# Kernel tuning notes

Measured on AMD Instinct MI355X. Metric: run time of the kernel, lower is better.

Reference implementation:

```python
import jax, jax.numpy as jnp
import numpy as np

EPS = 1e-5
SLOPE = 0.1


def _leaky(v):
    return jnp.where(v >= 0, v, SLOPE * v)


def _bn(v, gamma, beta):
    # v: (C, Q, k); training-mode batch norm over (Q, k) with biased variance
    m = v.mean(axis=(1, 2), keepdims=True)
    var = v.var(axis=(1, 2), keepdims=True)
    return (v - m) * jax.lax.rsqrt(var + EPS) * gamma[:, None, None] + beta[:, None, None]


def setup_inputs() -> dict:
    key = jax.random.key(0)
    ks = jax.random.split(key, 6)
    Q, S, K, F, O = 16384, 16384, 32, 64, 64
    q_points = jax.random.normal(ks[0], (Q, 3), dtype=jnp.float32)
    s_points = jax.random.normal(ks[1], (S, 3), dtype=jnp.float32)
    neighb_inds = jax.random.randint(ks[2], (Q, K), 0, S + 1)  # S is the padded zero row
    feat = jax.random.normal(ks[3], (S, F), dtype=jnp.float32)
    conv0_w = jax.random.normal(ks[4], (O, F), dtype=jnp.float32) * 0.1
    conv1_w = jax.random.normal(ks[5], (O * 3, O), dtype=jnp.float32) * 0.1
    return {
        "q_points": q_points,
        "s_points": s_points,
        "feat": feat,
        "neighb_inds": neighb_inds,
        "conv0_w": conv0_w,
        "gamma0": jnp.ones((O,), jnp.float32),
        "beta0": jnp.zeros((O,), jnp.float32),
        "conv1_w": conv1_w,
        "gamma1": jnp.ones((O,), jnp.float32),
        "beta1": jnp.zeros((O,), jnp.float32),
    }


def reference(q_points, s_points, feat, neighb_inds, conv0_w, gamma0, beta0, conv1_w, gamma1, beta1):
    Q, K = neighb_inds.shape
    n_supports = s_points.shape[0]
    out_c = conv1_w.shape[1]
    in_c = conv1_w.shape[0] // out_c  # = 3 for feat_mode='xyz'

    # pad with a zero row (index n_supports is the 'out of range' shadow point)
    s_pad = jnp.concatenate([s_points, jnp.zeros((1, s_points.shape[1]), s_points.dtype)], 0)
    f_pad = jnp.concatenate([feat, jnp.zeros((1, feat.shape[1]), feat.dtype)], 0)

    # relative xyz feature; zero out shadow neighbors
    x = s_pad[neighb_inds] - q_points[:, None, :]          # (Q, K, 3)
    mask = (neighb_inds == n_supports)[..., None]
    x = jnp.where(mask, jnp.zeros((), x.dtype), x)

    y = f_pad[neighb_inds]                                  # (Q, K, F)

    # kernel generation: conv0 (1x1) -> BN -> LeakyReLU -> conv1 (1x1)
    h = jnp.einsum('of,qkf->oqk', conv0_w, y)               # (O, Q, K)
    h = _leaky(_bn(h, gamma0, beta0))
    ker = jnp.einsum('co,oqk->qkc', conv1_w, h)             # (Q, K, O*in_c)
    ker = ker.reshape(Q, K, out_c, in_c)                    # (Q, K, O, 3)

    # per-edge matmul against relative xyz, then BN -> LeakyReLU -> max over k
    z = jnp.einsum('qkoi,qki->oqk', ker, x)                 # (O, Q, K)
    z = _leaky(_bn(z, gamma1, beta1))
    z = z.max(axis=2)                                       # (O, Q)
    return z.T                                              # (Q, O)
```

## Files before the change

### kernel.cpp

```cpp
#include <hip/hip_runtime.h>
#include <hip/hip_bf16.h>

typedef __attribute__((ext_vector_type(8))) short bf16x8;
typedef __attribute__((ext_vector_type(4))) float f32x4;

constexpr int Q = 16384, S = 16384, KNN = 32, F = 64, O = 64;
constexpr int NEDGE = Q * KNN;
constexpr int QB = 8;
constexpr int EB = 256;
constexpr int GD = Q / QB;
constexpr int GH = 256;
constexpr float EPSV = 1e-5f;

constexpr size_t CNT_OFF   = 0;
constexpr size_t CTR_OFF   = 65536;
constexpr size_t P0_OFF    = 65600;
constexpr size_t ST0_OFF   = P0_OFF + (size_t)GH * 128 * 4;
constexpr size_t ZMIN_OFF  = ST0_OFF + 512;
constexpr size_t P1_OFF    = ZMIN_OFF + (size_t)Q * O * 4;
constexpr size_t ST1_OFF   = P1_OFF + (size_t)GD * 128 * 4;
constexpr size_t W0F_OFF   = ST1_OFF + 512;
constexpr size_t W1F_OFF   = W0F_OFF + 8192;
constexpr size_t FEATB_OFF = W1F_OFF + 24576;

__device__ __forceinline__ short f2bf(float f) {
  __hip_bfloat16 h = __float2bfloat16(f);
  short r; __builtin_memcpy(&r, &h, 2); return r;
}

__global__ void k_prep_hist(const float* __restrict__ w0g, const float* __restrict__ w1g,
                            short* __restrict__ w0f, short* __restrict__ w1f,
                            const float* __restrict__ feat, short* __restrict__ featb,
                            const int* __restrict__ inds, int* __restrict__ cnt) {
  __shared__ int lh[S];
  const int bx = blockIdx.x, tt = threadIdx.x;
  if (bx < 8) {
    const int t = bx * 256 + tt;
    const int fa = t >> 6, ln = t & 63;
    const int l4 = ln >> 4, l15 = ln & 15;
    if (fa < 8) {
      const int mt = fa >> 1, kk = fa & 1;
      const int o = 16 * mt + l15, f = 32 * kk + 8 * l4;
      const float* src = w0g + o * 64 + f;
      bf16x8 pk;
#pragma unroll
      for (int j = 0; j < 8; ++j) pk[j] = f2bf(src[j]);
      *(bf16x8*)&w0f[t * 8] = pk;
    } else {
      const int fb = fa - 8;
      const int nt = fb >> 1, kk = fb & 1;
      const int i = nt >> 2, b = nt & 3;
      const int o = 16 * b + l15;
      const float* row = w1g + (o * 3 + i) * 64;
      const int base = 32 * kk + 4 * l4;
      bf16x8 pk;
#pragma unroll
      for (int j = 0; j < 4; ++j) pk[j] = f2bf(row[base + j]);
#pragma unroll
      for (int j = 4; j < 8; ++j) pk[j] = f2bf(row[base + 16 + (j & 3)]);
      *(bf16x8*)&w1f[(fb * 64 + ln) * 8] = pk;
    }
  } else if (bx < 72) {
    const int base = (bx - 8) * 16384;
#pragma unroll
    for (int j = 0; j < 8; ++j) {
      const int i = base + j * 2048 + tt * 8;
      f32x4 a = *(const f32x4*)(feat + i);
      f32x4 b = *(const f32x4*)(feat + i + 4);
      bf16x8 pk;
      pk[0] = f2bf(a[0]); pk[1] = f2bf(a[1]); pk[2] = f2bf(a[2]); pk[3] = f2bf(a[3]);
      pk[4] = f2bf(b[0]); pk[5] = f2bf(b[1]); pk[6] = f2bf(b[2]); pk[7] = f2bf(b[3]);
      *(bf16x8*)(featb + i) = pk;
    }
  } else {
    for (int c = tt; c < S; c += 256) lh[c] = 0;
    __syncthreads();
    const int4* ip = (const int4*)inds;
    const int base = (bx - 72) * 2048;
#pragma unroll
    for (int j = 0; j < 8; ++j) {
      const int4 v = ip[base + j * 256 + tt];
      if (v.x < S) atomicAdd(&lh[v.x], 1);
      if (v.y < S) atomicAdd(&lh[v.y], 1);
      if (v.z < S) atomicAdd(&lh[v.z], 1);
      if (v.w < S) atomicAdd(&lh[v.w], 1);
    }
    __syncthreads();
    for (int c = tt; c < S; c += 256) {
      const int v = lh[c];
      if (v) atomicAdd(&cnt[c], v);
    }
  }
}

__global__ void k_hsq(const short* __restrict__ featb, const int* __restrict__ cnt,
                      const short* __restrict__ w0f, float* __restrict__ p0,
                      int* __restrict__ ctr, const float* __restrict__ g0,
                      const float* __restrict__ b0, float* __restrict__ st0) {
  __shared__ float sred[4][2][64];
  __shared__ int isLast;
  const int t = threadIdx.x, blk = blockIdx.x;
  const int wv = t >> 6, ln = t & 63, l4 = ln >> 4, l15 = ln & 15;

  const bf16x8* w0v = (const bf16x8*)w0f;
  bf16x8 w0a[8];
#pragma unroll
  for (int fa = 0; fa < 8; ++fa) w0a[fa] = w0v[fa * 64 + ln];

  const int s0 = blk * 64 + wv * 16;
  const float wc = (float)cnt[s0 + l15];
  const short* fb = featb + (size_t)(s0 + l15) * F + 8 * l4;
  const bf16x8 y0 = *(const bf16x8*)(fb);
  const bf16x8 y1 = *(const bf16x8*)(fb + 32);

  float hs[4][4], hq[4][4];
#pragma unroll
  for (int mt = 0; mt < 4; ++mt) {
    f32x4 acc = {0.f, 0.f, 0.f, 0.f};
    acc = __builtin_amdgcn_mfma_f32_16x16x32_bf16(w0a[2 * mt], y0, acc, 0, 0, 0);
    acc = __builtin_amdgcn_mfma_f32_16x16x32_bf16(w0a[2 * mt + 1], y1, acc, 0, 0, 0);
#pragma unroll
    for (int r = 0; r < 4; ++r) {
      const float h = acc[r];
      hs[mt][r] = wc * h;
      hq[mt][r] = wc * h * h;
    }
  }
#pragma unroll
  for (int mt = 0; mt < 4; ++mt)
#pragma unroll
    for (int r = 0; r < 4; ++r) {
      float s = hs[mt][r], q = hq[mt][r];
#pragma unroll
      for (int d = 1; d < 16; d <<= 1) { s += __shfl_xor(s, d); q += __shfl_xor(q, d); }
      hs[mt][r] = s; hq[mt][r] = q;
    }
  if (l15 == 0) {
#pragma unroll
    for (int mt = 0; mt < 4; ++mt)
#pragma unroll
      for (int r = 0; r < 4; ++r) {
        const int o = 16 * mt + 4 * l4 + r;
        sred[wv][0][o] = hs[mt][r];
        sred[wv][1][o] = hq[mt][r];
      }
  }
  __syncthreads();
  if (t < 128) {
    const int qq = t >> 6, o = t & 63;
    p0[(size_t)blk * 128 + t] =
        sred[0][qq][o] + sred[1][qq][o] + sred[2][qq][o] + sred[3][qq][o];
  }
  __syncthreads();
  __threadfence();
  if (t == 0) isLast = (atomicAdd(&ctr[0], 1) == GH - 1);
  __syncthreads();
  if (isLast) {
    __threadfence();
    if (t < O) {
      float s = 0.f, q = 0.f;
      for (int b = 0; b < GH; ++b) {
        s += p0[(size_t)b * 128 + t];
        q += p0[(size_t)b * 128 + 64 + t];
      }
      const float invN = 1.f / (float)NEDGE;
      const float mean = s * invN;
      const float var = q * invN - mean * mean;
      const float sc = g0[t] * rsqrtf(var + EPSV);
      st0[t] = sc;
      st0[O + t] = b0[t] - mean * sc;
    }
  }
}

__launch_bounds__(256, 2)
__global__ void k_main(const float* __restrict__ qpts, const float* __restrict__ spts,
                       const short* __restrict__ featb, const int* __restrict__ inds,
                       const short* __restrict__ w0f, const short* __restrict__ w1f,
                       const float* __restrict__ st0,
                       float* __restrict__ zmax, float* __restrict__ zmin,
                       float* __restrict__ p1) {
  __shared__ __align__(16) float xs[3 * EB];
  __shared__ float swred[512];

  const int t = threadIdx.x, blk = blockIdx.x;
  const int wv = t >> 6, ln = t & 63, l4 = ln >> 4, l15 = ln & 15;
  const int ebase = blk * EB;

  const int idx0 = inds[ebase + t];
  {
    const int q = blk * QB + (t >> 5);
    float x0 = 0.f, x1 = 0.f, x2 = 0.f;
    if (idx0 < S) {
      x0 = spts[idx0 * 3 + 0] - qpts[q * 3 + 0];
      x1 = spts[idx0 * 3 + 1] - qpts[q * 3 + 1];
      x2 = spts[idx0 * 3 + 2] - qpts[q * 3 + 2];
    }
    xs[0 * EB + t] = x0; xs[1 * EB + t] = x1; xs[2 * EB + t] = x2;
  }

  int idxT[4];
#pragma unroll
  for (int nt = 0; nt < 4; ++nt) idxT[nt] = __shfl(idx0, nt * 16 + l15, 64);

  const bf16x8* w0v = (const bf16x8*)w0f;
  bf16x8 w0a[8];
#pragma unroll
  for (int fa = 0; fa < 8; ++fa) w0a[fa] = w0v[fa * 64 + ln];

  const float* scp = st0 + 4 * l4;
  const float* shp = st0 + O + 4 * l4;

  auto loadY = [&](int idx, bf16x8& y0, bf16x8& y1) {
    if (idx < S) {
      const short* fbp = featb + (size_t)idx * F + 8 * l4;
      y0 = *(const bf16x8*)(fbp);
      y1 = *(const bf16x8*)(fbp + 32);
    } else {
#pragma unroll
      for (int j = 0; j < 8; ++j) { y0[j] = 0; y1[j] = 0; }
    }
  };
  auto tileA = [&](const bf16x8& y0, const bf16x8& y1, bf16x8& h0, bf16x8& h1) {
#pragma unroll
    for (int kk = 0; kk < 2; ++kk) {
      f32x4 a0 = {0.f, 0.f, 0.f, 0.f}, a1 = {0.f, 0.f, 0.f, 0.f};
      a0 = __builtin_amdgcn_mfma_f32_16x16x32_bf16(w0a[4 * kk + 0], y0, a0, 0, 0, 0);
      a0 = __builtin_amdgcn_mfma_f32_16x16x32_bf16(w0a[4 * kk + 1], y1, a0, 0, 0, 0);
      a1 = __builtin_amdgcn_mfma_f32_16x16x32_bf16(w0a[4 * kk + 2], y0, a1, 0, 0, 0);
      a1 = __builtin_amdgcn_mfma_f32_16x16x32_bf16(w0a[4 * kk + 3], y1, a1, 0, 0, 0);
      const f32x4 sc0 = *(const f32x4*)(scp + 32 * kk);
      const f32x4 sh0 = *(const f32x4*)(shp + 32 * kk);
      const f32x4 sc1 = *(const f32x4*)(scp + 32 * kk + 16);
      const f32x4 sh1 = *(const f32x4*)(shp + 32 * kk + 16);
      bf16x8 h;
#pragma unroll
      for (int r = 0; r < 4; ++r) {
        float v = a0[r] * sc0[r] + sh0[r];
        v = fmaxf(v, 0.1f * v);
        h[r] = f2bf(v);
      }
#pragma unroll
      for (int r = 0; r < 4; ++r) {
        float v = a1[r] * sc1[r] + sh1[r];
        v = fmaxf(v, 0.1f * v);
        h[4 + r] = f2bf(v);
      }
      if (kk == 0) h0 = h; else h1 = h;
    }
  };

  bf16x8 hA[4][2];
  {
    bf16x8 ya0, ya1, yb0, yb1;
    loadY(idxT[0], ya0, ya1);
    loadY(idxT[1], yb0, yb1);
    tileA(ya0, ya1, hA[0][0], hA[0][1]);
    loadY(idxT[2], ya0, ya1);
    tileA(yb0, yb1, hA[1][0], hA[1][1]);
    loadY(idxT[3], yb0, yb1);
    tileA(ya0, ya1, hA[2][0], hA[2][1]);
    tileA(yb0, yb1, hA[3][0], hA[3][1]);
  }

  const bf16x8* w1v = (const bf16x8*)w1f;
  float zmx[2][4], zmn[2][4], zs[4], zq[4];
#pragma unroll
  for (int j = 0; j < 4; ++j) {
    zs[j] = 0.f; zq[j] = 0.f;
    zmx[0][j] = -3.4e38f; zmx[1][j] = -3.4e38f;
    zmn[0][j] = 3.4e38f;  zmn[1][j] = 3.4e38f;
  }

#pragma unroll
  for (int b = 0; b < 4; ++b) {
    bf16x8 w1b[6];
#pragma unroll
    for (int i = 0; i < 3; ++i)
#pragma unroll
      for (int kk = 0; kk < 2; ++kk)
        w1b[i * 2 + kk] = w1v[(((i * 4 + b) * 2) + kk) * 64 + ln];
#pragma unroll
    for (int mt = 0; mt < 4; ++mt) {
      const int ex = wv * 64 + mt * 16 + 4 * l4;
      f32x4 z4 = {0.f, 0.f, 0.f, 0.f};
#pragma unroll
      for (int i = 0; i < 3; ++i) {
        f32x4 acc = {0.f, 0.f, 0.f, 0.f};
        acc = __builtin_amdgcn_mfma_f32_16x16x32_bf16(hA[mt][0], w1b[2 * i], acc, 0, 0, 0);
        acc = __builtin_amdgcn_mfma_f32_16x16x32_bf16(hA[mt][1], w1b[2 * i + 1], acc, 0, 0, 0);
        const f32x4 xv = *(const f32x4*)&xs[i * EB + ex];
#pragma unroll
        for (int r = 0; r < 4; ++r) z4[r] += acc[r] * xv[r];
      }
      const int qh = mt >> 1;
#pragma unroll
      for (int r = 0; r < 4; ++r) {
        const float v = z4[r];
        zmx[qh][b] = fmaxf(zmx[qh][b], v);
        zmn[qh][b] = fminf(zmn[qh][b], v);
        zs[b] += v; zq[b] += v * v;
      }
    }
  }

#pragma unroll
  for (int qh = 0; qh < 2; ++qh)
#pragma unroll
    for (int b = 0; b < 4; ++b) {
      float m = zmx[qh][b];
      m = fmaxf(m, __shfl_xor(m, 16)); m = fmaxf(m, __shfl_xor(m, 32));
      zmx[qh][b] = m;
      float n = zmn[qh][b];
      n = fminf(n, __shfl_xor(n, 16)); n = fminf(n, __shfl_xor(n, 32));
      zmn[qh][b] = n;
    }
#pragma unroll
  for (int b = 0; b < 4; ++b) {
    float s = zs[b];  s += __shfl_xor(s, 16);  s += __shfl_xor(s, 32);  zs[b] = s;
    float sq = zq[b]; sq += __shfl_xor(sq, 16); sq += __shfl_xor(sq, 32); zq[b] = sq;
  }

  if (l4 == 0) {
#pragma unroll
    for (int qh = 0; qh < 2; ++qh) {
      const int q = blk * QB + wv * 2 + qh;
#pragma unroll
      for (int b = 0; b < 4; ++b) {
        zmax[(size_t)q * O + 16 * b + l15] = zmx[qh][b];
        zmin[(size_t)q * O + 16 * b + l15] = zmn[qh][b];
      }
    }
#pragma unroll
    for (int b = 0; b < 4; ++b) {
      swred[wv * 128 + 16 * b + l15] = zs[b];
      swred[wv * 128 + 64 + 16 * b + l15] = zq[b];
    }
  }
  __syncthreads();
  if (t < 128)
    p1[(size_t)blk * 128 + t] = swred[t] + swred[128 + t] + swred[256 + t] + swred[384 + t];
}

__global__ void k_red1(const float* __restrict__ p1, const float* __restrict__ g1,
                       const float* __restrict__ b1, float* __restrict__ st1) {
  __shared__ float rs[256], rq[256];
  const int o = blockIdx.x, t = threadIdx.x;
  float s = 0.f, q = 0.f;
  for (int r = t; r < GD; r += 256) {
    s += p1[(size_t)r * 128 + o];
    q += p1[(size_t)r * 128 + 64 + o];
  }
  rs[t] = s; rq[t] = q;
  __syncthreads();
  for (int off = 128; off > 0; off >>= 1) {
    if (t < off) { rs[t] += rs[t + off]; rq[t] += rq[t + off]; }
    __syncthreads();
  }
  if (t == 0) {
    const float invN = 1.f / (float)NEDGE;
    const float mean = rs[0] * invN;
    const float var = rq[0] * invN - mean * mean;
    const float sc = g1[o] * rsqrtf(var + EPSV);
    st1[o] = sc;
    st1[O + o] = b1[o] - mean * sc;
  }
}

__global__ void k_final(const float* __restrict__ st1, const float* __restrict__ zmin,
                        float* __restrict__ out) {
  const int i4 = blockIdx.x * blockDim.x + threadIdx.x;
  const int o0 = (i4 * 4) & 63;
  const f32x4 mx = *(const f32x4*)(out + (size_t)i4 * 4);
  const f32x4 mn = *(const f32x4*)(zmin + (size_t)i4 * 4);
  const f32x4 sc = *(const f32x4*)(st1 + o0);
  const f32x4 sh = *(const f32x4*)(st1 + O + o0);
  f32x4 r;
#pragma unroll
  for (int j = 0; j < 4; ++j) {
    const float base = (sc[j] >= 0.f) ? mx[j] : mn[j];
    const float v = base * sc[j] + sh[j];
    r[j] = fmaxf(v, 0.1f * v);
  }
  *(f32x4*)(out + (size_t)i4 * 4) = r;
}

extern "C" void kernel_launch(void* const* d_in, const int* in_sizes, int n_in,
                              void* d_out, int out_size, void* d_ws, size_t ws_size,
                              hipStream_t stream) {
  const float* qpts = (const float*)d_in[0];
  const float* spts = (const float*)d_in[1];
  const float* feat = (const float*)d_in[2];
  const int*   inds = (const int*)d_in[3];
  const float* w0   = (const float*)d_in[4];
  const float* g0   = (const float*)d_in[5];
  const float* b0   = (const float*)d_in[6];
  const float* w1   = (const float*)d_in[7];
  const float* g1   = (const float*)d_in[8];
  const float* b1   = (const float*)d_in[9];
  float* out = (float*)d_out;

  char* ws = (char*)d_ws;
  int*   cnt   = (int*)(ws + CNT_OFF);
  int*   ctr   = (int*)(ws + CTR_OFF);
  float* p0    = (float*)(ws + P0_OFF);
  float* st0   = (float*)(ws + ST0_OFF);
  float* zmin  = (float*)(ws + ZMIN_OFF);
  float* p1    = (float*)(ws + P1_OFF);
  float* st1   = (float*)(ws + ST1_OFF);
  short* w0f   = (short*)(ws + W0F_OFF);
  short* w1f   = (short*)(ws + W1F_OFF);
  short* featb = (short*)(ws + FEATB_OFF);

  hipMemsetAsync(ws, 0, CTR_OFF + 64, stream);
  k_prep_hist<<<136, 256, 0, stream>>>(w0, w1, w0f, w1f, feat, featb, inds, cnt);
  k_hsq<<<GH, 256, 0, stream>>>(featb, cnt, w0f, p0, ctr, g0, b0, st0);
  k_main<<<GD, 256, 0, stream>>>(qpts, spts, featb, inds, w0f, w1f, st0, out, zmin, p1);
  k_red1<<<64, 256, 0, stream>>>(p1, g1, b1, st1);
  k_final<<<(Q * O) / 1024, 256, 0, stream>>>(st1, zmin, out);
}
```

Baseline: 87.99 us.

## Shrink main kernel to single-wave blocks and split BN1 reduction into two stages

The main kernel now runs one 64-thread wave per block, handling two queries, instead of four waves per block. This drops the shared-memory block reduction and the __syncthreads, and each wave writes its partial sums straight to global memory. The final BN statistics are reduced in two kernels: 512 blocks sum groups of 16 partials, then one block finishes. The histogram-weighted stats kernel now processes 256 support points per block with 64 blocks, and the memset is replaced by a small zeroing kernel. The trade-off is 8192 tiny blocks with more global partial traffic and one extra launch.

```diff
diff --git a/kernel.cpp b/kernel.cpp
--- a/kernel.cpp
+++ b/kernel.cpp
@@ -3,13 +3,12 @@
 
 typedef __attribute__((ext_vector_type(8))) short bf16x8;
 typedef __attribute__((ext_vector_type(4))) float f32x4;
+typedef __attribute__((ext_vector_type(4))) int i32x4;
 
 constexpr int Q = 16384, S = 16384, KNN = 32, F = 64, O = 64;
 constexpr int NEDGE = Q * KNN;
-constexpr int QB = 8;
-constexpr int EB = 256;
-constexpr int GD = Q / QB;
-constexpr int GH = 256;
+constexpr int GD2 = Q / 2;
+constexpr int GH = 64;
 constexpr float EPSV = 1e-5f;
 
 constexpr size_t CNT_OFF   = 0;
@@ -18,7 +17,8 @@
 constexpr size_t ST0_OFF   = P0_OFF + (size_t)GH * 128 * 4;
 constexpr size_t ZMIN_OFF  = ST0_OFF + 512;
 constexpr size_t P1_OFF    = ZMIN_OFF + (size_t)Q * O * 4;
-constexpr size_t ST1_OFF   = P1_OFF + (size_t)GD * 128 * 4;
+constexpr size_t P2_OFF    = P1_OFF + (size_t)GD2 * 128 * 4;
+constexpr size_t ST1_OFF   = P2_OFF + (size_t)512 * 128 * 4;
 constexpr size_t W0F_OFF   = ST1_OFF + 512;
 constexpr size_t W1F_OFF   = W0F_OFF + 8192;
 constexpr size_t FEATB_OFF = W1F_OFF + 24576;
@@ -26,6 +26,14 @@
 __device__ __forceinline__ short f2bf(float f) {
   __hip_bfloat16 h = __float2bfloat16(f);
   short r; __builtin_memcpy(&r, &h, 2); return r;
+}
+
+__global__ void k_zero(int* __restrict__ p) {
+  const int i4 = blockIdx.x * 256 + threadIdx.x;
+  if (i4 < 4100) {
+    i32x4 z = {0, 0, 0, 0};
+    *(i32x4*)(p + i4 * 4) = z;
+  }
 }
 
 __global__ void k_prep_hist(const float* __restrict__ w0g, const float* __restrict__ w1g,
@@ -107,23 +115,30 @@
 #pragma unroll
   for (int fa = 0; fa < 8; ++fa) w0a[fa] = w0v[fa * 64 + ln];
 
-  const int s0 = blk * 64 + wv * 16;
-  const float wc = (float)cnt[s0 + l15];
-  const short* fb = featb + (size_t)(s0 + l15) * F + 8 * l4;
-  const bf16x8 y0 = *(const bf16x8*)(fb);
-  const bf16x8 y1 = *(const bf16x8*)(fb + 32);
-
   float hs[4][4], hq[4][4];
 #pragma unroll
-  for (int mt = 0; mt < 4; ++mt) {
-    f32x4 acc = {0.f, 0.f, 0.f, 0.f};
-    acc = __builtin_amdgcn_mfma_f32_16x16x32_bf16(w0a[2 * mt], y0, acc, 0, 0, 0);
-    acc = __builtin_amdgcn_mfma_f32_16x16x32_bf16(w0a[2 * mt + 1], y1, acc, 0, 0, 0);
-#pragma unroll
-    for (int r = 0; r < 4; ++r) {
-      const float h = acc[r];
-      hs[mt][r] = wc * h;
-      hq[mt][r] = wc * h * h;
+  for (int mt = 0; mt < 4; ++mt)
+#pragma unroll
+    for (int r = 0; r < 4; ++r) { hs[mt][r] = 0.f; hq[mt][r] = 0.f; }
+
+#pragma unroll
+  for (int tile = 0; tile < 4; ++tile) {
+    const int s0 = blk * 256 + wv * 64 + tile * 16;
+    const float wc = (float)cnt[s0 + l15];
+    const short* fb = featb + (size_t)(s0 + l15) * F + 8 * l4;
+    const bf16x8 y0 = *(const bf16x8*)(fb);
+    const bf16x8 y1 = *(const bf16x8*)(fb + 32);
+#pragma unroll
+    for (int mt = 0; mt < 4; ++mt) {
+      f32x4 acc = {0.f, 0.f, 0.f, 0.f};
+      acc = __builtin_amdgcn_mfma_f32_16x16x32_bf16(w0a[2 * mt], y0, acc, 0, 0, 0);
+      acc = __builtin_amdgcn_mfma_f32_16x16x32_bf16(w0a[2 * mt + 1], y1, acc, 0, 0, 0);
+#pragma unroll
+      for (int r = 0; r < 4; ++r) {
+        const float h = acc[r];
+        hs[mt][r] += wc * h;
+        hq[mt][r] += wc * h * h;
+      }
     }
   }
 #pragma unroll
@@ -173,30 +188,29 @@
   }
 }
 
-__launch_bounds__(256, 2)
+__launch_bounds__(64, 3)
 __global__ void k_main(const float* __restrict__ qpts, const float* __restrict__ spts,
                        const short* __restrict__ featb, const int* __restrict__ inds,
                        const short* __restrict__ w0f, const short* __restrict__ w1f,
                        const float* __restrict__ st0,
                        float* __restrict__ zmax, float* __restrict__ zmin,
                        float* __restrict__ p1) {
-  __shared__ __align__(16) float xs[3 * EB];
-  __shared__ float swred[512];
+  __shared__ __align__(16) float xs[3 * 64];
 
   const int t = threadIdx.x, blk = blockIdx.x;
-  const int wv = t >> 6, ln = t & 63, l4 = ln >> 4, l15 = ln & 15;
-  const int ebase = blk * EB;
+  const int l4 = t >> 4, l15 = t & 15;
+  const int ebase = blk * 64;
 
   const int idx0 = inds[ebase + t];
   {
-    const int q = blk * QB + (t >> 5);
+    const int q = blk * 2 + (t >> 5);
     float x0 = 0.f, x1 = 0.f, x2 = 0.f;
     if (idx0 < S) {
       x0 = spts[idx0 * 3 + 0] - qpts[q * 3 + 0];
       x1 = spts[idx0 * 3 + 1] - qpts[q * 3 + 1];
       x2 = spts[idx0 * 3 + 2] - qpts[q * 3 + 2];
     }
-    xs[0 * EB + t] = x0; xs[1 * EB + t] = x1; xs[2 * EB + t] = x2;
+    xs[0 * 64 + t] = x0; xs[1 * 64 + t] = x1; xs[2 * 64 + t] = x2;
   }
 
   int idxT[4];
@@ -206,7 +220,7 @@
   const bf16x8* w0v = (const bf16x8*)w0f;
   bf16x8 w0a[8];
 #pragma unroll
-  for (int fa = 0; fa < 8; ++fa) w0a[fa] = w0v[fa * 64 + ln];
+  for (int fa = 0; fa < 8; ++fa) w0a[fa] = w0v[fa * 64 + t];
 
   const float* scp = st0 + 4 * l4;
   const float* shp = st0 + O + 4 * l4;
@@ -279,17 +293,17 @@
     for (int i = 0; i < 3; ++i)
 #pragma unroll
       for (int kk = 0; kk < 2; ++kk)
-        w1b[i * 2 + kk] = w1v[(((i * 4 + b) * 2) + kk) * 64 + ln];
+        w1b[i * 2 + kk] = w1v[(((i * 4 + b) * 2) + kk) * 64 + t];
 #pragma unroll
     for (int mt = 0; mt < 4; ++mt) {
-      const int ex = wv * 64 + mt * 16 + 4 * l4;
+      const int ex = mt * 16 + 4 * l4;
       f32x4 z4 = {0.f, 0.f, 0.f, 0.f};
 #pragma unroll
       for (int i = 0; i < 3; ++i) {
         f32x4 acc = {0.f, 0.f, 0.f, 0.f};
         acc = __builtin_amdgcn_mfma_f32_16x16x32_bf16(hA[mt][0], w1b[2 * i], acc, 0, 0, 0);
         acc = __builtin_amdgcn_mfma_f32_16x16x32_bf16(hA[mt][1], w1b[2 * i + 1], acc, 0, 0, 0);
-        const f32x4 xv = *(const f32x4*)&xs[i * EB + ex];
+        const f32x4 xv = *(const f32x4*)&xs[i * 64 + ex];
 #pragma unroll
         for (int r = 0; r < 4; ++r) z4[r] += acc[r] * xv[r];
       }
@@ -324,7 +338,7 @@
   if (l4 == 0) {
 #pragma unroll
     for (int qh = 0; qh < 2; ++qh) {
-      const int q = blk * QB + wv * 2 + qh;
+      const int q = blk * 2 + qh;
 #pragma unroll
       for (int b = 0; b < 4; ++b) {
         zmax[(size_t)q * O + 16 * b + l15] = zmx[qh][b];
@@ -333,37 +347,38 @@
     }
 #pragma unroll
     for (int b = 0; b < 4; ++b) {
-      swred[wv * 128 + 16 * b + l15] = zs[b];
-      swred[wv * 128 + 64 + 16 * b + l15] = zq[b];
-    }
-  }
+      p1[(size_t)blk * 128 + 16 * b + l15] = zs[b];
+      p1[(size_t)blk * 128 + 64 + 16 * b + l15] = zq[b];
+    }
+  }
+}
+
+__global__ void k_red1a(const float* __restrict__ p1, float* __restrict__ p2) {
+  const int t = threadIdx.x;
+  const int b = blockIdx.x;
+  const float* base = p1 + (size_t)b * 16 * 128;
+  float s = 0.f;
+#pragma unroll
+  for (int r = 0; r < 16; ++r) s += base[r * 128 + t];
+  p2[(size_t)b * 128 + t] = s;
+}
+
+__global__ void k_red1b(const float* __restrict__ p2, const float* __restrict__ g1,
+                        const float* __restrict__ b1, float* __restrict__ st1) {
+  __shared__ float red[128];
+  const int t = threadIdx.x;
+  float s = 0.f;
+#pragma unroll 4
+  for (int r = 0; r < 512; ++r) s += p2[(size_t)r * 128 + t];
+  red[t] = s;
   __syncthreads();
-  if (t < 128)
-    p1[(size_t)blk * 128 + t] = swred[t] + swred[128 + t] + swred[256 + t] + swred[384 + t];
-}
-
-__global__ void k_red1(const float* __restrict__ p1, const float* __restrict__ g1,
-                       const float* __restrict__ b1, float* __restrict__ st1) {
-  __shared__ float rs[256], rq[256];
-  const int o = blockIdx.x, t = threadIdx.x;
-  float s = 0.f, q = 0.f;
-  for (int r = t; r < GD; r += 256) {
-    s += p1[(size_t)r * 128 + o];
-    q += p1[(size_t)r * 128 + 64 + o];
-  }
-  rs[t] = s; rq[t] = q;
-  __syncthreads();
-  for (int off = 128; off > 0; off >>= 1) {
-    if (t < off) { rs[t] += rs[t + off]; rq[t] += rq[t + off]; }
-    __syncthreads();
-  }
-  if (t == 0) {
+  if (t < O) {
     const float invN = 1.f / (float)NEDGE;
-    const float mean = rs[0] * invN;
-    const float var = rq[0] * invN - mean * mean;
-    const float sc = g1[o] * rsqrtf(var + EPSV);
-    st1[o] = sc;
-    st1[O + o] = b1[o] - mean * sc;
+    const float mean = red[t] * invN;
+    const float var = red[64 + t] * invN - mean * mean;
+    const float sc = g1[t] * rsqrtf(var + EPSV);
+    st1[t] = sc;
+    st1[O + t] = b1[t] - mean * sc;
   }
 }
 
@@ -407,15 +422,17 @@
   float* st0   = (float*)(ws + ST0_OFF);
   float* zmin  = (float*)(ws + ZMIN_OFF);
   float* p1    = (float*)(ws + P1_OFF);
+  float* p2    = (float*)(ws + P2_OFF);
   float* st1   = (float*)(ws + ST1_OFF);
   short* w0f   = (short*)(ws + W0F_OFF);
   short* w1f   = (short*)(ws + W1F_OFF);
   short* featb = (short*)(ws + FEATB_OFF);
 
-  hipMemsetAsync(ws, 0, CTR_OFF + 64, stream);
+  k_zero<<<17, 256, 0, stream>>>(cnt);
   k_prep_hist<<<136, 256, 0, stream>>>(w0, w1, w0f, w1f, feat, featb, inds, cnt);
   k_hsq<<<GH, 256, 0, stream>>>(featb, cnt, w0f, p0, ctr, g0, b0, st0);
-  k_main<<<GD, 256, 0, stream>>>(qpts, spts, featb, inds, w0f, w1f, st0, out, zmin, p1);
-  k_red1<<<64, 256, 0, stream>>>(p1, g1, b1, st1);
+  k_main<<<GD2, 64, 0, stream>>>(qpts, spts, featb, inds, w0f, w1f, st0, out, zmin, p1);
+  k_red1a<<<512, 128, 0, stream>>>(p1, p2);
+  k_red1b<<<1, 128, 0, stream>>>(p2, g1, b1, st1);
   k_final<<<(Q * O) / 1024, 256, 0, stream>>>(st1, zmin, out);
 }
```

Measured after the change: 101.3 us. 15.1% more time.
